# Performance work log

Hardware: AMD Instinct MI355X
Metric: run time of the kernel (lower is better)

## Reference

```python
import jax, jax.numpy as jnp
import numpy as np

N_BITS = 16
BATCH = 4194304  # 2**22 tokens
TABLE_SIZE = 2 ** (N_BITS - 1)  # largest CUMULATIVE/FLIP context is n_bits-1 bits


def setup_inputs() -> dict:
    key = jax.random.key(0)
    k1, k2 = jax.random.split(key)
    # input bit tensor [batch, n_bits], values in {0,1}; index n_bits-1 is bit 0 (LSB)
    bits = jax.random.randint(k1, (BATCH, N_BITS), 0, 2, dtype=jnp.int32)
    # per-bit-position RAM lookup tables, padded to the max address space.
    # Binary contents {0,1}, stored as float32 so the flip/XOR math is expressible.
    tables = (jax.random.uniform(k2, (N_BITS, TABLE_SIZE)) < 0.5).astype(jnp.float32)
    return {"bits": bits, "tables": tables}


def reference(bits, tables):
    """BitLevelMapper forward, CUMULATIVE context + FLIP output mode.

    bits:   [B, n_bits] int32 in {0,1}, array index n_bits-1-k holds bit value k (LSB=k=0)
    tables: [n_bits, 2^(n_bits-1)] float32 in {0,1}; row i is the RAM/LUT for bit_pos i.
    For bit_pos i the context is the lowest i bits (bit0..bit_{i-1});
    address = sum_k context_bit_k * 2^k; flip = table[i, address];
    output bit i = input bit i XOR flip.
    """
    n_bits = bits.shape[1]
    bits_rev = bits[:, ::-1]                      # [B, n] column k = bit value k
    k = jnp.arange(n_bits)
    # W[i, k] = 2^k if k < i else 0  -> addr_i = sum_{k<i} bit_k * 2^k (addr_0 = 0)
    W = jnp.where(k[None, :] < k[:, None], (1 << k)[None, :], 0).astype(jnp.int32)
    addr = bits_rev @ W.T                          # [B, n] int32 RAM addresses per bit_pos
    flip = tables[k[None, :], addr]                # [B, n] gather: tables[i, addr[b, i]]
    x = bits_rev.astype(tables.dtype)
    out_rev = x + flip - 2.0 * x * flip            # XOR expressed arithmetically
    return out_rev[:, ::-1]                        # back to original bit-array layout
```

## Files before the change

### kernel.cpp

```cpp
#include <hip/hip_runtime.h>
#include <hip/hip_bf16.h>


#define PACK_WORDS 2048

typedef float vfloat4 __attribute__((ext_vector_type(4)));

__global__ __launch_bounds__(256) void
pack_tables_kernel(const float* __restrict__ tables, unsigned* __restrict__ packed) {
    int g = blockIdx.x * blockDim.x + threadIdx.x;
    bool val = false;
    if (g < 65535) {
        int i = 31 - __clz(g + 1);
        int a = g - ((1 << i) - 1);
        val = tables[i * 32768 + a] != 0.0f;
    }
    unsigned long long m = __ballot(val);
    if ((threadIdx.x & 63) == 0) {
        packed[(g >> 5)]     = (unsigned)m;
        packed[(g >> 5) + 1] = (unsigned)(m >> 32);
    }
}

__device__ __forceinline__ unsigned nib(const int4& m) {
    return (unsigned)((m.x << 3) | (m.y << 2) | (m.z << 1) | m.w);
}

__device__ __forceinline__ void
process_chunk(unsigned pk, const unsigned* __restrict__ tab,
              vfloat4* __restrict__ out4, size_t base, int lane) {
    const int hi   = lane >> 4;
    const int bsrc = (lane & 15) << 2;
    unsigned v = 0;
    #pragma unroll
    for (int q = 0; q < 4; ++q) {
        unsigned x  = (unsigned)__shfl((int)pk, bsrc + q, 64);
        unsigned nb = (x >> (hi * 4)) & 0xFu;
        v |= nb << (12 - 4 * q);
    }

    unsigned r16 = 0;
    #pragma unroll
    for (int i = 0; i < 16; ++i) {
        unsigned mask = (1u << i) - 1u;
        unsigned bidx = mask + (v & mask);
        unsigned fl   = (tab[bidx >> 5] >> (bidx & 31u));
        r16 |= (((v >> i) ^ fl) & 1u) << i;
    }

    #pragma unroll
    for (int j = 0; j < 4; ++j) {
        unsigned y = (unsigned)__shfl((int)r16, (j << 4) + (lane >> 2), 64);
        int q4 = (lane & 3) << 2;
        vfloat4 f;
        f.x = (float)((y >> (15 - q4)) & 1u);
        f.y = (float)((y >> (14 - q4)) & 1u);
        f.z = (float)((y >> (13 - q4)) & 1u);
        f.w = (float)((y >> (12 - q4)) & 1u);
        __builtin_nontemporal_store(f, &out4[base + j * 64 + lane]);
    }
}

__global__ __launch_bounds__(256) void
blm_kernel(const int4* __restrict__ bits4, const unsigned* __restrict__ packed,
           vfloat4* __restrict__ out4, int nrows) {
    __shared__ unsigned tab[PACK_WORDS];
    for (int k = threadIdx.x; k < PACK_WORDS; k += 256)
        tab[k] = packed[k];
    __syncthreads();

    const int lane    = threadIdx.x & 63;
    const int wave    = (blockIdx.x * 256 + threadIdx.x) >> 6;
    const int nwaves  = (gridDim.x * 256) >> 6;
    const int npairs  = nrows >> 7;

    for (int p = wave; p < npairs; p += nwaves) {
        const size_t base = (size_t)p * 512;

        int4 a0 = bits4[base +   0 + lane];
        int4 a1 = bits4[base +  64 + lane];
        int4 a2 = bits4[base + 128 + lane];
        int4 a3 = bits4[base + 192 + lane];
        int4 b0 = bits4[base + 256 + lane];
        int4 b1 = bits4[base + 320 + lane];
        int4 b2 = bits4[base + 384 + lane];
        int4 b3 = bits4[base + 448 + lane];

        unsigned pkA = nib(a0) | (nib(a1) << 4) | (nib(a2) << 8) | (nib(a3) << 12);
        unsigned pkB = nib(b0) | (nib(b1) << 4) | (nib(b2) << 8) | (nib(b3) << 12);

        process_chunk(pkA, tab, out4, base,       lane);
        process_chunk(pkB, tab, out4, base + 256, lane);
    }
}

extern "C" void kernel_launch(void* const* d_in, const int* in_sizes, int n_in,
                              void* d_out, int out_size, void* d_ws, size_t ws_size,
                              hipStream_t stream) {
    const int*   bits   = (const int*)d_in[0];
    const float* tables = (const float*)d_in[1];
    float*       out    = (float*)d_out;
    unsigned*    packed = (unsigned*)d_ws;

    int nrows = in_sizes[0] / 16;

    pack_tables_kernel<<<65536 / 256, 256, 0, stream>>>(tables, packed);

    blm_kernel<<<8192, 256, 0, stream>>>((const int4*)bits, packed,
                                         (vfloat4*)out, nrows);
}
```

Before: 451.1 us.

## Software-pipeline input loads across grid-stride chunks and shrink grid

Reworks the main loop so each wave processes one 64-row chunk per iteration and prefetches the next chunk's bits into registers while processing the current one. The grid shrinks from 8192 to 1024 blocks, so each wave does more iterations and the shared-table fill is amortized over more rows. The table copy into LDS now uses 16-byte vector loads. The aim is to hide global load latency for this bandwidth-bound kernel, at the cost of fewer resident waves and extra registers for the prefetch buffers.

```diff
diff --git a/kernel.cpp b/kernel.cpp
--- a/kernel.cpp
+++ b/kernel.cpp
@@ -65,32 +65,46 @@
 blm_kernel(const int4* __restrict__ bits4, const unsigned* __restrict__ packed,
            vfloat4* __restrict__ out4, int nrows) {
     __shared__ unsigned tab[PACK_WORDS];
-    for (int k = threadIdx.x; k < PACK_WORDS; k += 256)
-        tab[k] = packed[k];
+    {
+        const int4* p4 = (const int4*)packed;
+        int4* t4 = (int4*)tab;
+        for (int k = threadIdx.x; k < PACK_WORDS / 4; k += 256)
+            t4[k] = p4[k];
+    }
     __syncthreads();
 
     const int lane    = threadIdx.x & 63;
     const int wave    = (blockIdx.x * 256 + threadIdx.x) >> 6;
     const int nwaves  = (gridDim.x * 256) >> 6;
-    const int npairs  = nrows >> 7;
+    const int nchunks = nrows >> 6;
 
-    for (int p = wave; p < npairs; p += nwaves) {
-        const size_t base = (size_t)p * 512;
+    int c = wave;
+    if (c >= nchunks) return;
 
-        int4 a0 = bits4[base +   0 + lane];
-        int4 a1 = bits4[base +  64 + lane];
-        int4 a2 = bits4[base + 128 + lane];
-        int4 a3 = bits4[base + 192 + lane];
-        int4 b0 = bits4[base + 256 + lane];
-        int4 b1 = bits4[base + 320 + lane];
-        int4 b2 = bits4[base + 384 + lane];
-        int4 b3 = bits4[base + 448 + lane];
+    size_t base = (size_t)c * 256;
+    int4 m0 = bits4[base +   0 + lane];
+    int4 m1 = bits4[base +  64 + lane];
+    int4 m2 = bits4[base + 128 + lane];
+    int4 m3 = bits4[base + 192 + lane];
 
-        unsigned pkA = nib(a0) | (nib(a1) << 4) | (nib(a2) << 8) | (nib(a3) << 12);
-        unsigned pkB = nib(b0) | (nib(b1) << 4) | (nib(b2) << 8) | (nib(b3) << 12);
+    while (true) {
+        int cn = c + nwaves;
+        int4 n0, n1, n2, n3;
+        bool have_next = cn < nchunks;
+        if (have_next) {
+            size_t nb = (size_t)cn * 256;
+            n0 = bits4[nb +   0 + lane];
+            n1 = bits4[nb +  64 + lane];
+            n2 = bits4[nb + 128 + lane];
+            n3 = bits4[nb + 192 + lane];
+        }
 
-        process_chunk(pkA, tab, out4, base,       lane);
-        process_chunk(pkB, tab, out4, base + 256, lane);
+        unsigned pk = nib(m0) | (nib(m1) << 4) | (nib(m2) << 8) | (nib(m3) << 12);
+        process_chunk(pk, tab, out4, base, lane);
+
+        if (!have_next) break;
+        m0 = n0; m1 = n1; m2 = n2; m3 = n3;
+        c = cn; base = (size_t)c * 256;
     }
 }
 
@@ -106,6 +120,6 @@
 
     pack_tables_kernel<<<65536 / 256, 256, 0, stream>>>(tables, packed);
 
-    blm_kernel<<<8192, 256, 0, stream>>>((const int4*)bits, packed,
+    blm_kernel<<<1024, 256, 0, stream>>>((const int4*)bits, packed,
                                          (vfloat4*)out, nrows);
 }
```

Result: no change. 449.8 us (-0.3%).
